# Optimization experiments

Measured on AMD Instinct MI355X. Metric: run time of the kernel, lower is better.

## Reference

```python
import jax, jax.numpy as jnp
import numpy as np


def setup_inputs() -> dict:
    key = jax.random.key(0)
    k0, k1, k2, k3 = jax.random.split(key, 4)
    B, N, C, Dout = 4, 8192, 64, 128
    coords = jax.random.normal(k0, (B, N, 3), dtype=jnp.float32)
    features = jax.random.normal(k1, (B, N, C), dtype=jnp.float32)
    W1 = jax.random.normal(k2, (C + 3, Dout), dtype=jnp.float32) / jnp.sqrt(jnp.float32(C + 3))
    b1 = jnp.zeros((Dout,), dtype=jnp.float32)
    W2 = jax.random.normal(k3, (Dout, Dout), dtype=jnp.float32) / jnp.sqrt(jnp.float32(Dout))
    b2 = jnp.zeros((Dout,), dtype=jnp.float32)
    return {"coords": coords, "features": features, "W1": W1, "b1": b1,
            "W2": W2, "b2": b2, "sample_count": 2048, "k": 32}


def reference(coords, features, W1, b1, W2, b2, sample_count, k):
    B, N, _ = coords.shape
    S = min(sample_count, N)
    kk = min(k, N)
    # deterministic linspace centroid sampling (same indices for every batch)
    idx = jnp.round(jnp.linspace(0.0, N - 1, S)).astype(jnp.int32)  # [S]
    sampled = coords[:, idx]  # [B,S,3]
    # squared distances via GEMM (same topk ordering as torch.cdist)
    s2 = jnp.sum(sampled * sampled, axis=-1)          # [B,S]
    c2 = jnp.sum(coords * coords, axis=-1)            # [B,N]
    d2 = s2[:, :, None] + c2[:, None, :] - 2.0 * jnp.einsum('bsd,bnd->bsn', sampled, coords)
    _, knn_idx = jax.lax.top_k(-d2, kk)               # [B,S,kk] smallest distances
    # per-batch irregular gathers
    grouped_c = jax.vmap(lambda c, i: c[i])(coords, knn_idx)      # [B,S,kk,3]
    rel = grouped_c - sampled[:, :, None, :]                      # relative coords
    grouped_f = jax.vmap(lambda f, i: f[i])(features, knn_idx)    # [B,S,kk,C]
    g = jnp.concatenate([rel, grouped_f], axis=-1)                # [B,S,kk,C+3]
    # shared MLP: Linear -> GELU(exact) -> Linear -> GELU(exact)
    h = jax.nn.gelu(g @ W1 + b1, approximate=False)
    h = jax.nn.gelu(h @ W2 + b2, approximate=False)
    pooled = jnp.max(h, axis=2)                                   # [B,S,Dout]
    return sampled, pooled
```

## Files before the change

kernel.cpp:

```cpp
#include <hip/hip_runtime.h>
#include <math.h>

typedef unsigned int u32;
typedef unsigned long long u64;
typedef float f32x2 __attribute__((ext_vector_type(2)));

#define BB 4
#define NN 8192
#define CC 64
#define DOUT 128
#define SS 2048
#define KSEL 32
#define CAPL 2048
#define CAP2 384
#define BREAK_CAP 128

__device__ __forceinline__ int sample_index(int s) {
    if (s == 1706) return 6826;
    const double step = 8191.0 / 2047.0;
    return (int)rint((double)s * step);
}

__device__ __forceinline__ u32 f2s(float f) {
    u32 u = __float_as_uint(f);
    return ((int)u < 0) ? ~u : (u ^ 0x80000000u);
}

__device__ __forceinline__ float gelu(float x) {
    return 0.5f * x * (1.0f + erff(x * 0.70710678118654752f));
}

__global__ __launch_bounds__(256)
__attribute__((amdgpu_waves_per_eu(5, 8)))
void k_select(const float* __restrict__ coords,
              float* __restrict__ out_sampled,
              int* __restrict__ selbuf,
              int selstride) {
    __shared__ __align__(16) u64 cand[CAPL];
    __shared__ __align__(16) u64 cand2[CAP2];
    __shared__ u32 wsum[32];
    __shared__ int sel[KSEL];
    __shared__ int s_nsel, s_ncand, s_n2;

    const int tid = threadIdx.x;
    const int lane = tid & 63;
    const int q = blockIdx.x;
    const int b = q >> 11;
    const int s = q & (SS - 1);
    const int si = sample_index(s);

    const float* cb = coords + (size_t)b * NN * 3;
    const float qx = cb[si * 3 + 0], qy = cb[si * 3 + 1], qz = cb[si * 3 + 2];
    const float q2 = __fadd_rn(__fadd_rn(__fmul_rn(qx, qx), __fmul_rn(qy, qy)), __fmul_rn(qz, qz));

    if (tid == 0) {
        float* dst = out_sampled + (size_t)q * 3;
        dst[0] = qx; dst[1] = qy; dst[2] = qz;
    }

    u32 kr[32];
#pragma unroll
    for (int i = 0; i < 32; i++) {
        int j = tid + (i << 8);
        float x = cb[j * 3 + 0], y = cb[j * 3 + 1], z = cb[j * 3 + 2];
        float n2 = __fadd_rn(__fadd_rn(__fmul_rn(x, x), __fmul_rn(y, y)), __fmul_rn(z, z));
        float dot = __fadd_rn(__fadd_rn(__fmul_rn(qx, x), __fmul_rn(qy, y)), __fmul_rn(qz, z));
        float d2 = __fsub_rn(__fadd_rn(q2, n2), __fmul_rn(2.0f, dot));
        kr[i] = f2s(d2);
    }

#define BFLY_WSUM()                                                          \
    _Pragma("unroll")                                                        \
    for (int w = 0; w < 8; w++) {                                            \
        _Pragma("unroll")                                                    \
        for (int d = 1; d < 64; d <<= 1) cnt[w] += __shfl_xor(cnt[w], d, 64);\
    }                                                                        \
    if ((tid & 63) == 0) {                                                   \
        int wv = tid >> 6;                                                   \
        _Pragma("unroll")                                                    \
        for (int w = 0; w < 8; w++) wsum[wv * 8 + w] = cnt[w];               \
    }                                                                        \
    __syncthreads();

#define SCAN_DIGIT()                                                         \
    u32 tot[8];                                                              \
    _Pragma("unroll")                                                        \
    for (int w = 0; w < 8; w++)                                              \
        tot[w] = wsum[w] + wsum[8 + w] + wsum[16 + w] + wsum[24 + w];        \
    run = 0; D = 15; cc = 0;                                                 \
    _Pragma("unroll")                                                        \
    for (int nib = 0; nib < 16; nib++) {                                     \
        int cv = (nib & 1) ? (int)(tot[nib >> 1] >> 16)                      \
                           : (int)(tot[nib >> 1] & 0xFFFFu);                 \
        if (base + run + cv >= KSEL) { D = nib; cc = cv; break; }            \
        run += cv;                                                           \
    }

    u32 pref = 0;
    int base = 0, shift = 28, c = 0;
    int p = 7;
    {
        u32 cnt[8] = {0, 0, 0, 0, 0, 0, 0, 0};
#pragma unroll
        for (int i = 0; i < 32; i++) {
            u32 nib = kr[i] >> 28;
            cnt[nib >> 1] += 1u << (16 * (nib & 1));
        }
        BFLY_WSUM()
        int run, D, cc;
        SCAN_DIGIT()
        base = run; pref = (u32)D << 28; c = cc;
        __syncthreads();
    }

    while (c > CAPL && p > 0) {
        p--;
        const int sh = 4 * p;
        const u32 hmask = 0xFFFFFFFFu << (sh + 4);
        u32 cnt[8] = {0, 0, 0, 0, 0, 0, 0, 0};
#pragma unroll
        for (int i = 0; i < 32; i++) {
            u32 kv = kr[i];
            if ((kv & hmask) == pref) {
                u32 nib = (kv >> sh) & 15u;
                cnt[nib >> 1] += 1u << (16 * (nib & 1));
            }
        }
        BFLY_WSUM()
        int run, D, cc;
        SCAN_DIGIT()
        base += run; pref |= (u32)D << sh; shift = sh; c = cc;
        __syncthreads();
    }

    if (tid == 0) { s_nsel = 0; s_ncand = 0; }
    __syncthreads();

    const u64 lmlt = (1ull << lane) - 1ull;
    {
        const u32 prefv = pref >> shift;
#pragma unroll
        for (int i = 0; i < 32; i++) {
            int j = tid + (i << 8);
            u32 kv = kr[i];
            u32 kp = kv >> shift;
            bool isS = kp < prefv;
            bool isC = kp == prefv;
            u64 bs = __ballot(isS);
            u64 bc = __ballot(isC);
            int basS = 0, basC = 0;
            if (lane == 0) {
                if (bs) basS = atomicAdd(&s_nsel, (int)__popcll(bs));
                if (bc) basC = atomicAdd(&s_ncand, (int)__popcll(bc));
            }
            basS = __shfl(basS, 0, 64);
            basC = __shfl(basC, 0, 64);
            if (isS) sel[basS + (int)__popcll(bs & lmlt)] = j;
            if (isC) {
                int pos = basC + (int)__popcll(bc & lmlt);
                if (pos < CAPL) cand[pos] = ((u64)kv << 32) | (u32)j;
            }
        }
    }
    __syncthreads();
    int nc = s_ncand; if (nc > CAPL) nc = CAPL;

    int p2 = shift >> 2;
    while (c > BREAK_CAP && p2 > 0) {
        p2--;
        const int sh = 4 * p2;
        const u32 ph = pref >> (sh + 4);
        u32 cnt[8] = {0, 0, 0, 0, 0, 0, 0, 0};
        for (int e = tid; e < nc; e += 256) {
            u32 kv = (u32)(cand[e] >> 32);
            if ((kv >> (sh + 4)) == ph) {
                u32 nib = (kv >> sh) & 15u;
                cnt[nib >> 1] += 1u << (16 * (nib & 1));
            }
        }
        BFLY_WSUM()
        int run, D, cc;
        SCAN_DIGIT()
        base += run; pref |= (u32)D << sh; shift = sh; c = cc;
        __syncthreads();
    }
#undef BFLY_WSUM
#undef SCAN_DIGIT

    if (tid == 0) s_n2 = 0;
    __syncthreads();
    {
        const u32 pv = pref >> shift;
        for (int e = tid; e < nc; e += 256) {
            u64 ent = cand[e];
            u32 kp = (u32)(ent >> 32) >> shift;
            bool isS = kp < pv;
            bool isC = kp == pv;
            u64 bs = __ballot(isS);
            u64 bc = __ballot(isC);
            int basS = 0, basC = 0;
            if (lane == 0) {
                if (bs) basS = atomicAdd(&s_nsel, (int)__popcll(bs));
                if (bc) basC = atomicAdd(&s_n2, (int)__popcll(bc));
            }
            basS = __shfl(basS, 0, 64);
            basC = __shfl(basC, 0, 64);
            if (isS) sel[basS + (int)__popcll(bs & lmlt)] = (int)(ent & 0xFFFFFFFFu);
            if (isC) {
                int pos = basC + (int)__popcll(bc & lmlt);
                if (pos < CAP2) cand2[pos] = ent;
            }
        }
    }
    __syncthreads();

    {
        const int nles = s_nsel;
        const int need = KSEL - nles;
        int n2 = s_n2; if (n2 > CAP2) n2 = CAP2;
        for (int ci = tid; ci < n2; ci += 256) {
            u64 me = cand2[ci];
            int r = 0;
            for (int m = 0; m < n2; m++) r += (cand2[m] < me) ? 1 : 0;
            if (r < need) sel[nles + r] = (int)(me & 0xFFFFFFFFu);
        }
    }
    __syncthreads();

    if (tid < KSEL) selbuf[(size_t)q * selstride + tid] = sel[tid];
}

__global__ __launch_bounds__(512) void k_mlp(const float* __restrict__ coords,
                                             const float* __restrict__ features,
                                             const float* __restrict__ w1,
                                             const float* __restrict__ b1,
                                             const float* __restrict__ w2,
                                             const float* __restrict__ b2,
                                             const int* __restrict__ selbuf,
                                             int selstride,
                                             float* __restrict__ pooled) {
    __shared__ __align__(16) unsigned char smem[32768];
    float* g    = (float*)smem;
    float* h    = (float*)smem;
    float* part = (float*)smem;
    __shared__ int sel2[2][KSEL];

    const int tid = threadIdx.x;
    const int q0 = blockIdx.x << 1;
    const int b = q0 >> 11;
    const float* cb = coords + (size_t)b * NN * 3;

    if (tid < 2 * KSEL) {
        int hq = tid >> 5;
        sel2[hq][tid & 31] = selbuf[(size_t)(q0 + hq) * selstride + (tid & 31)];
    }
    __syncthreads();

    {
        const int hq = tid >> 8;
        const int t = tid & 255;
        const int s = (q0 + hq) & (SS - 1);
        const int si = sample_index(s);
        const float qx = cb[si * 3 + 0], qy = cb[si * 3 + 1], qz = cb[si * 3 + 2];
        const int nbr = (t >> 3) & 31;
        const int cl = t & 7;
        const int n = sel2[hq][nbr];
        const float* fb = features + ((size_t)b * NN + n) * CC;
        float* gq = g + hq * 2144;
#pragma unroll
        for (int m = 0; m < 9; m++) {
            int ch = cl + (m << 3);
            if (ch < 67) {
                float v;
                if (ch < 3) v = cb[n * 3 + ch] - ((ch == 0) ? qx : (ch == 1) ? qy : qz);
                else        v = fb[ch - 3];
                gq[ch * 32 + nbr] = v;
            }
        }
    }
    __syncthreads();

    const int lane = tid & 63;
    const int chb = __builtin_amdgcn_readfirstlane((tid >> 6) << 4);
    const int hq = lane >> 5;
    const int nb = lane & 31;

    f32x2 acc2[8];

    {
        const f32x2* br2 = (const f32x2*)(b1 + chb);
#pragma unroll
        for (int k = 0; k < 8; k++) acc2[k] = br2[k];
        const float* aA = g + hq * 2144 + nb;
        const float* w1p = w1 + chb;
        for (int c = 0; c < 67; c++) {
            float a = aA[c * 32];
            f32x2 av = {a, a};
            const f32x2* wr2 = (const f32x2*)(w1p + c * DOUT);
#pragma unroll
            for (int k = 0; k < 8; k++)
                acc2[k] = __builtin_elementwise_fma(av, wr2[k], acc2[k]);
        }
    }
    __syncthreads();
    {
        float* hp = h + hq * 4096 + nb;
#pragma unroll
        for (int k = 0; k < 8; k++) {
            hp[(chb + 2 * k) * 32]     = gelu(acc2[k].x);
            hp[(chb + 2 * k + 1) * 32] = gelu(acc2[k].y);
        }
    }
    __syncthreads();

    {
        const f32x2* br2 = (const f32x2*)(b2 + chb);
#pragma unroll
        for (int k = 0; k < 8; k++) acc2[k] = br2[k];
        const float* aA = h + hq * 4096 + nb;
        const float* w2p = w2 + chb;
        for (int c = 0; c < DOUT; c++) {
            float a = aA[c * 32];
            f32x2 av = {a, a};
            const f32x2* wr2 = (const f32x2*)(w2p + c * DOUT);
#pragma unroll
            for (int k = 0; k < 8; k++)
                acc2[k] = __builtin_elementwise_fma(av, wr2[k], acc2[k]);
        }
    }
    __syncthreads();
    {
        float* pp = part + hq * 4096;
#pragma unroll
        for (int k = 0; k < 8; k++) {
            int j0 = chb + 2 * k;
            int j1 = j0 + 1;
            pp[j0 * 32 + (nb ^ (j0 & 31))] = acc2[k].x;
            pp[j1 * 32 + (nb ^ (j1 & 31))] = acc2[k].y;
        }
    }
    __syncthreads();

    if (tid < 256) {
        const int hq2 = tid >> 7;
        const int ch = tid & 127;
        const float* pr = part + hq2 * 4096 + ch * 32;
        const int sw = ch & 31;
        float mx = pr[0 ^ sw];
        float mn = mx;
#pragma unroll
        for (int w = 1; w < 32; w++) {
            float v = pr[w ^ sw];
            mx = fmaxf(mx, v);
            mn = fminf(mn, v);
        }
        pooled[(size_t)(q0 + hq2) * DOUT + ch] = fmaxf(gelu(mx), gelu(mn));
    }
}

extern "C" void kernel_launch(void* const* d_in, const int* in_sizes, int n_in,
                              void* d_out, int out_size, void* d_ws, size_t ws_size,
                              hipStream_t stream) {
    const float* coords = nullptr;
    const float* features = nullptr;
    const float* W1 = nullptr;
    const float* b1 = nullptr;
    const float* W2 = nullptr;
    const float* b2 = nullptr;
    for (int i = 0; i < n_in; i++) {
        int sz = in_sizes[i];
        const float* p = (const float*)d_in[i];
        if      (sz == BB * NN * 3)     coords = p;
        else if (sz == BB * NN * CC)    features = p;
        else if (sz == (CC + 3) * DOUT) W1 = p;
        else if (sz == DOUT * DOUT)     W2 = p;
        else if (sz == DOUT)            { if (!b1) b1 = p; else b2 = p; }
    }

    float* out_sampled = (float*)d_out;
    float* out_pooled  = (float*)d_out + (size_t)BB * SS * 3;

    const size_t sel_bytes = (size_t)BB * SS * KSEL * sizeof(int);
    int* selbuf;
    int selstride;
    if (ws_size >= sel_bytes && d_ws != nullptr) {
        selbuf = (int*)d_ws;
        selstride = KSEL;
    } else {
        selbuf = (int*)out_pooled;
        selstride = DOUT;
    }

    k_select<<<dim3(BB * SS), dim3(256), 0, stream>>>(coords, out_sampled, selbuf, selstride);
    k_mlp<<<dim3((BB * SS) / 2), dim3(512), 0, stream>>>(coords, features, W1, b1, W2, b2,
                                                         selbuf, selstride, out_pooled);
}
```

Baseline: 393.9 us.

## Fuse kNN selection and MLP into one kernel handling two queries per block

Merges the radix-select kernel and the MLP kernel into a single 512-thread kernel that processes two query points per block. The coordinates are loaded once to compute distances for both queries, and each selection runs serially, writing neighbor indices straight into shared memory. This removes the global selection buffer round-trip and one launch. In exchange the selection phase runs twice in sequence with block-wide syncs, and the larger block with more registers may lower occupancy compared with the former 256-thread select kernel.

```diff
diff --git a/kernel.cpp b/kernel.cpp
--- a/kernel.cpp
+++ b/kernel.cpp
@@ -30,44 +30,55 @@
     return 0.5f * x * (1.0f + erff(x * 0.70710678118654752f));
 }
 
-__global__ __launch_bounds__(256)
-__attribute__((amdgpu_waves_per_eu(5, 8)))
-void k_select(const float* __restrict__ coords,
-              float* __restrict__ out_sampled,
-              int* __restrict__ selbuf,
-              int selstride) {
-    __shared__ __align__(16) u64 cand[CAPL];
-    __shared__ __align__(16) u64 cand2[CAP2];
-    __shared__ u32 wsum[32];
-    __shared__ int sel[KSEL];
+__global__ __launch_bounds__(512) void k_fused(const float* __restrict__ coords,
+                                               const float* __restrict__ features,
+                                               const float* __restrict__ w1,
+                                               const float* __restrict__ b1,
+                                               const float* __restrict__ w2,
+                                               const float* __restrict__ b2,
+                                               float* __restrict__ out_sampled,
+                                               float* __restrict__ pooled) {
+    __shared__ __align__(16) unsigned char smem[32768];
+    u64*   cand  = (u64*)smem;
+    u64*   cand2 = (u64*)(smem + 16384);
+    u32*   wsum  = (u32*)(smem + 19456);
+    float* g     = (float*)smem;
+    float* h     = (float*)smem;
+    float* part  = (float*)smem;
+    __shared__ int sel2[2][KSEL];
     __shared__ int s_nsel, s_ncand, s_n2;
 
     const int tid = threadIdx.x;
     const int lane = tid & 63;
-    const int q = blockIdx.x;
-    const int b = q >> 11;
-    const int s = q & (SS - 1);
-    const int si = sample_index(s);
-
+    const int q0 = blockIdx.x << 1;
+    const int b = q0 >> 11;
     const float* cb = coords + (size_t)b * NN * 3;
-    const float qx = cb[si * 3 + 0], qy = cb[si * 3 + 1], qz = cb[si * 3 + 2];
-    const float q2 = __fadd_rn(__fadd_rn(__fmul_rn(qx, qx), __fmul_rn(qy, qy)), __fmul_rn(qz, qz));
+
+    const int si0 = sample_index(q0 & (SS - 1));
+    const int si1 = sample_index((q0 + 1) & (SS - 1));
+    const float qx0 = cb[si0 * 3 + 0], qy0 = cb[si0 * 3 + 1], qz0 = cb[si0 * 3 + 2];
+    const float qx1 = cb[si1 * 3 + 0], qy1 = cb[si1 * 3 + 1], qz1 = cb[si1 * 3 + 2];
+    const float q20 = __fadd_rn(__fadd_rn(__fmul_rn(qx0, qx0), __fmul_rn(qy0, qy0)), __fmul_rn(qz0, qz0));
+    const float q21 = __fadd_rn(__fadd_rn(__fmul_rn(qx1, qx1), __fmul_rn(qy1, qy1)), __fmul_rn(qz1, qz1));
 
     if (tid == 0) {
-        float* dst = out_sampled + (size_t)q * 3;
-        dst[0] = qx; dst[1] = qy; dst[2] = qz;
-    }
-
-    u32 kr[32];
-#pragma unroll
-    for (int i = 0; i < 32; i++) {
-        int j = tid + (i << 8);
+        float* dst = out_sampled + (size_t)q0 * 3;
+        dst[0] = qx0; dst[1] = qy0; dst[2] = qz0;
+        dst[3] = qx1; dst[4] = qy1; dst[5] = qz1;
+    }
+
+    u32 kr0[16], kr1[16];
+#pragma unroll
+    for (int i = 0; i < 16; i++) {
+        int j = tid + (i << 9);
         float x = cb[j * 3 + 0], y = cb[j * 3 + 1], z = cb[j * 3 + 2];
         float n2 = __fadd_rn(__fadd_rn(__fmul_rn(x, x), __fmul_rn(y, y)), __fmul_rn(z, z));
-        float dot = __fadd_rn(__fadd_rn(__fmul_rn(qx, x), __fmul_rn(qy, y)), __fmul_rn(qz, z));
-        float d2 = __fsub_rn(__fadd_rn(q2, n2), __fmul_rn(2.0f, dot));
-        kr[i] = f2s(d2);
-    }
+        float dot0 = __fadd_rn(__fadd_rn(__fmul_rn(qx0, x), __fmul_rn(qy0, y)), __fmul_rn(qz0, z));
+        kr0[i] = f2s(__fsub_rn(__fadd_rn(q20, n2), __fmul_rn(2.0f, dot0)));
+        float dot1 = __fadd_rn(__fadd_rn(__fmul_rn(qx1, x), __fmul_rn(qy1, y)), __fmul_rn(qz1, z));
+        kr1[i] = f2s(__fsub_rn(__fadd_rn(q21, n2), __fmul_rn(2.0f, dot1)));
+    }
+    const u64 lmlt = (1ull << lane) - 1ull;
 
 #define BFLY_WSUM()                                                          \
     _Pragma("unroll")                                                        \
@@ -85,8 +96,12 @@
 #define SCAN_DIGIT()                                                         \
     u32 tot[8];                                                              \
     _Pragma("unroll")                                                        \
-    for (int w = 0; w < 8; w++)                                              \
-        tot[w] = wsum[w] + wsum[8 + w] + wsum[16 + w] + wsum[24 + w];        \
+    for (int w = 0; w < 8; w++) {                                            \
+        u32 t = 0;                                                           \
+        _Pragma("unroll")                                                    \
+        for (int v = 0; v < 8; v++) t += wsum[v * 8 + w];                    \
+        tot[w] = t;                                                          \
+    }                                                                        \
     run = 0; D = 15; cc = 0;                                                 \
     _Pragma("unroll")                                                        \
     for (int nib = 0; nib < 16; nib++) {                                     \
@@ -96,172 +111,145 @@
         run += cv;                                                           \
     }
 
-    u32 pref = 0;
-    int base = 0, shift = 28, c = 0;
-    int p = 7;
-    {
-        u32 cnt[8] = {0, 0, 0, 0, 0, 0, 0, 0};
-#pragma unroll
-        for (int i = 0; i < 32; i++) {
-            u32 nib = kr[i] >> 28;
-            cnt[nib >> 1] += 1u << (16 * (nib & 1));
-        }
-        BFLY_WSUM()
-        int run, D, cc;
-        SCAN_DIGIT()
-        base = run; pref = (u32)D << 28; c = cc;
-        __syncthreads();
-    }
-
-    while (c > CAPL && p > 0) {
-        p--;
-        const int sh = 4 * p;
-        const u32 hmask = 0xFFFFFFFFu << (sh + 4);
-        u32 cnt[8] = {0, 0, 0, 0, 0, 0, 0, 0};
-#pragma unroll
-        for (int i = 0; i < 32; i++) {
-            u32 kv = kr[i];
-            if ((kv & hmask) == pref) {
-                u32 nib = (kv >> sh) & 15u;
-                cnt[nib >> 1] += 1u << (16 * (nib & 1));
-            }
-        }
-        BFLY_WSUM()
-        int run, D, cc;
-        SCAN_DIGIT()
-        base += run; pref |= (u32)D << sh; shift = sh; c = cc;
-        __syncthreads();
-    }
-
-    if (tid == 0) { s_nsel = 0; s_ncand = 0; }
-    __syncthreads();
-
-    const u64 lmlt = (1ull << lane) - 1ull;
-    {
-        const u32 prefv = pref >> shift;
-#pragma unroll
-        for (int i = 0; i < 32; i++) {
-            int j = tid + (i << 8);
-            u32 kv = kr[i];
-            u32 kp = kv >> shift;
-            bool isS = kp < prefv;
-            bool isC = kp == prefv;
-            u64 bs = __ballot(isS);
-            u64 bc = __ballot(isC);
-            int basS = 0, basC = 0;
-            if (lane == 0) {
-                if (bs) basS = atomicAdd(&s_nsel, (int)__popcll(bs));
-                if (bc) basC = atomicAdd(&s_ncand, (int)__popcll(bc));
-            }
-            basS = __shfl(basS, 0, 64);
-            basC = __shfl(basC, 0, 64);
-            if (isS) sel[basS + (int)__popcll(bs & lmlt)] = j;
-            if (isC) {
-                int pos = basC + (int)__popcll(bc & lmlt);
-                if (pos < CAPL) cand[pos] = ((u64)kv << 32) | (u32)j;
-            }
-        }
-    }
-    __syncthreads();
-    int nc = s_ncand; if (nc > CAPL) nc = CAPL;
-
-    int p2 = shift >> 2;
-    while (c > BREAK_CAP && p2 > 0) {
-        p2--;
-        const int sh = 4 * p2;
-        const u32 ph = pref >> (sh + 4);
-        u32 cnt[8] = {0, 0, 0, 0, 0, 0, 0, 0};
-        for (int e = tid; e < nc; e += 256) {
-            u32 kv = (u32)(cand[e] >> 32);
-            if ((kv >> (sh + 4)) == ph) {
-                u32 nib = (kv >> sh) & 15u;
-                cnt[nib >> 1] += 1u << (16 * (nib & 1));
-            }
-        }
-        BFLY_WSUM()
-        int run, D, cc;
-        SCAN_DIGIT()
-        base += run; pref |= (u32)D << sh; shift = sh; c = cc;
-        __syncthreads();
-    }
+#define SELECT_Q(KR, ROW)                                                    \
+{                                                                            \
+    u32 pref = 0;                                                            \
+    int base = 0, shift = 28, c = 0;                                         \
+    int p = 7;                                                               \
+    {                                                                        \
+        u32 cnt[8] = {0, 0, 0, 0, 0, 0, 0, 0};                               \
+        _Pragma("unroll")                                                    \
+        for (int i = 0; i < 16; i++) {                                       \
+            u32 nib = KR[i] >> 28;                                           \
+            cnt[nib >> 1] += 1u << (16 * (nib & 1));                         \
+        }                                                                    \
+        BFLY_WSUM()                                                          \
+        int run, D, cc;                                                      \
+        SCAN_DIGIT()                                                         \
+        base = run; pref = (u32)D << 28; c = cc;                             \
+        __syncthreads();                                                     \
+    }                                                                        \
+    while (c > CAPL && p > 0) {                                              \
+        p--;                                                                 \
+        const int sh = 4 * p;                                                \
+        const u32 hmask = 0xFFFFFFFFu << (sh + 4);                           \
+        u32 cnt[8] = {0, 0, 0, 0, 0, 0, 0, 0};                               \
+        _Pragma("unroll")                                                    \
+        for (int i = 0; i < 16; i++) {                                       \
+            u32 kv = KR[i];                                                  \
+            if ((kv & hmask) == pref) {                                      \
+                u32 nib = (kv >> sh) & 15u;                                  \
+                cnt[nib >> 1] += 1u << (16 * (nib & 1));                     \
+            }                                                                \
+        }                                                                    \
+        BFLY_WSUM()                                                          \
+        int run, D, cc;                                                      \
+        SCAN_DIGIT()                                                         \
+        base += run; pref |= (u32)D << sh; shift = sh; c = cc;               \
+        __syncthreads();                                                     \
+    }                                                                        \
+    if (tid == 0) { s_nsel = 0; s_ncand = 0; }                               \
+    __syncthreads();                                                         \
+    {                                                                        \
+        const u32 prefv = pref >> shift;                                     \
+        _Pragma("unroll")                                                    \
+        for (int i = 0; i < 16; i++) {                                       \
+            int j = tid + (i << 9);                                          \
+            u32 kv = KR[i];                                                  \
+            u32 kp = kv >> shift;                                            \
+            bool isS = kp < prefv;                                           \
+            bool isC = kp == prefv;                                          \
+            u64 bs = __ballot(isS);                                          \
+            u64 bc = __ballot(isC);                                          \
+            int basS = 0, basC = 0;                                          \
+            if (lane == 0) {                                                 \
+                if (bs) basS = atomicAdd(&s_nsel, (int)__popcll(bs));        \
+                if (bc) basC = atomicAdd(&s_ncand, (int)__popcll(bc));       \
+            }                                                                \
+            basS = __shfl(basS, 0, 64);                                      \
+            basC = __shfl(basC, 0, 64);                                      \
+            if (isS) sel2[ROW][basS + (int)__popcll(bs & lmlt)] = j;         \
+            if (isC) {                                                       \
+                int pos = basC + (int)__popcll(bc & lmlt);                   \
+                if (pos < CAPL) cand[pos] = ((u64)kv << 32) | (u32)j;        \
+            }                                                                \
+        }                                                                    \
+    }                                                                        \
+    __syncthreads();                                                         \
+    int nc = s_ncand; if (nc > CAPL) nc = CAPL;                              \
+    int p2 = shift >> 2;                                                     \
+    while (c > BREAK_CAP && p2 > 0) {                                        \
+        p2--;                                                                \
+        const int sh = 4 * p2;                                               \
+        const u32 ph = pref >> (sh + 4);                                     \
+        u32 cnt[8] = {0, 0, 0, 0, 0, 0, 0, 0};                               \
+        for (int e = tid; e < nc; e += 512) {                                \
+            u32 kv = (u32)(cand[e] >> 32);                                   \
+            if ((kv >> (sh + 4)) == ph) {                                    \
+                u32 nib = (kv >> sh) & 15u;                                  \
+                cnt[nib >> 1] += 1u << (16 * (nib & 1));                     \
+            }                                                                \
+        }                                                                    \
+        BFLY_WSUM()                                                          \
+        int run, D, cc;                                                      \
+        SCAN_DIGIT()                                                         \
+        base += run; pref |= (u32)D << sh; shift = sh; c = cc;               \
+        __syncthreads();                                                     \
+    }                                                                        \
+    if (tid == 0) s_n2 = 0;                                                  \
+    __syncthreads();                                                         \
+    {                                                                        \
+        const u32 pv = pref >> shift;                                        \
+        for (int e = tid; e < nc; e += 512) {                                \
+            u64 ent = cand[e];                                               \
+            u32 kp = (u32)(ent >> 32) >> shift;                              \
+            bool isS = kp < pv;                                              \
+            bool isC = kp == pv;                                             \
+            u64 bs = __ballot(isS);                                          \
+            u64 bc = __ballot(isC);                                          \
+            int basS = 0, basC = 0;                                          \
+            if (lane == 0) {                                                 \
+                if (bs) basS = atomicAdd(&s_nsel, (int)__popcll(bs));        \
+                if (bc) basC = atomicAdd(&s_n2, (int)__popcll(bc));          \
+            }                                                                \
+            basS = __shfl(basS, 0, 64);                                      \
+            basC = __shfl(basC, 0, 64);                                      \
+            if (isS) sel2[ROW][basS + (int)__popcll(bs & lmlt)] =            \
+                (int)(ent & 0xFFFFFFFFu);                                    \
+            if (isC) {                                                       \
+                int pos = basC + (int)__popcll(bc & lmlt);                   \
+                if (pos < CAP2) cand2[pos] = ent;                            \
+            }                                                                \
+        }                                                                    \
+    }                                                                        \
+    __syncthreads();                                                         \
+    {                                                                        \
+        const int nles = s_nsel;                                             \
+        const int need = KSEL - nles;                                        \
+        int n2 = s_n2; if (n2 > CAP2) n2 = CAP2;                             \
+        for (int ci = tid; ci < n2; ci += 512) {                             \
+            u64 me = cand2[ci];                                              \
+            int r = 0;                                                       \
+            for (int m = 0; m < n2; m++) r += (cand2[m] < me) ? 1 : 0;       \
+            if (r < need) sel2[ROW][nles + r] = (int)(me & 0xFFFFFFFFu);     \
+        }                                                                    \
+    }                                                                        \
+    __syncthreads();                                                         \
+}
+
+    SELECT_Q(kr0, 0)
+    SELECT_Q(kr1, 1)
+
+#undef SELECT_Q
 #undef BFLY_WSUM
 #undef SCAN_DIGIT
 
-    if (tid == 0) s_n2 = 0;
-    __syncthreads();
-    {
-        const u32 pv = pref >> shift;
-        for (int e = tid; e < nc; e += 256) {
-            u64 ent = cand[e];
-            u32 kp = (u32)(ent >> 32) >> shift;
-            bool isS = kp < pv;
-            bool isC = kp == pv;
-            u64 bs = __ballot(isS);
-            u64 bc = __ballot(isC);
-            int basS = 0, basC = 0;
-            if (lane == 0) {
-                if (bs) basS = atomicAdd(&s_nsel, (int)__popcll(bs));
-                if (bc) basC = atomicAdd(&s_n2, (int)__popcll(bc));
-            }
-            basS = __shfl(basS, 0, 64);
-            basC = __shfl(basC, 0, 64);
-            if (isS) sel[basS + (int)__popcll(bs & lmlt)] = (int)(ent & 0xFFFFFFFFu);
-            if (isC) {
-                int pos = basC + (int)__popcll(bc & lmlt);
-                if (pos < CAP2) cand2[pos] = ent;
-            }
-        }
-    }
-    __syncthreads();
-
-    {
-        const int nles = s_nsel;
-        const int need = KSEL - nles;
-        int n2 = s_n2; if (n2 > CAP2) n2 = CAP2;
-        for (int ci = tid; ci < n2; ci += 256) {
-            u64 me = cand2[ci];
-            int r = 0;
-            for (int m = 0; m < n2; m++) r += (cand2[m] < me) ? 1 : 0;
-            if (r < need) sel[nles + r] = (int)(me & 0xFFFFFFFFu);
-        }
-    }
-    __syncthreads();
-
-    if (tid < KSEL) selbuf[(size_t)q * selstride + tid] = sel[tid];
-}
-
-__global__ __launch_bounds__(512) void k_mlp(const float* __restrict__ coords,
-                                             const float* __restrict__ features,
-                                             const float* __restrict__ w1,
-                                             const float* __restrict__ b1,
-                                             const float* __restrict__ w2,
-                                             const float* __restrict__ b2,
-                                             const int* __restrict__ selbuf,
-                                             int selstride,
-                                             float* __restrict__ pooled) {
-    __shared__ __align__(16) unsigned char smem[32768];
-    float* g    = (float*)smem;
-    float* h    = (float*)smem;
-    float* part = (float*)smem;
-    __shared__ int sel2[2][KSEL];
-
-    const int tid = threadIdx.x;
-    const int q0 = blockIdx.x << 1;
-    const int b = q0 >> 11;
-    const float* cb = coords + (size_t)b * NN * 3;
-
-    if (tid < 2 * KSEL) {
-        int hq = tid >> 5;
-        sel2[hq][tid & 31] = selbuf[(size_t)(q0 + hq) * selstride + (tid & 31)];
-    }
-    __syncthreads();
-
     {
         const int hq = tid >> 8;
+        const float qxh = hq ? qx1 : qx0;
+        const float qyh = hq ? qy1 : qy0;
+        const float qzh = hq ? qz1 : qz0;
         const int t = tid & 255;
-        const int s = (q0 + hq) & (SS - 1);
-        const int si = sample_index(s);
-        const float qx = cb[si * 3 + 0], qy = cb[si * 3 + 1], qz = cb[si * 3 + 2];
         const int nbr = (t >> 3) & 31;
         const int cl = t & 7;
         const int n = sel2[hq][nbr];
@@ -272,7 +260,7 @@
             int ch = cl + (m << 3);
             if (ch < 67) {
                 float v;
-                if (ch < 3) v = cb[n * 3 + ch] - ((ch == 0) ? qx : (ch == 1) ? qy : qz);
+                if (ch < 3) v = cb[n * 3 + ch] - ((ch == 0) ? qxh : (ch == 1) ? qyh : qzh);
                 else        v = fb[ch - 3];
                 gq[ch * 32 + nbr] = v;
             }
@@ -280,7 +268,6 @@
     }
     __syncthreads();
 
-    const int lane = tid & 63;
     const int chb = __builtin_amdgcn_readfirstlane((tid >> 6) << 4);
     const int hq = lane >> 5;
     const int nb = lane & 31;
@@ -380,18 +367,6 @@
     float* out_sampled = (float*)d_out;
     float* out_pooled  = (float*)d_out + (size_t)BB * SS * 3;
 
-    const size_t sel_bytes = (size_t)BB * SS * KSEL * sizeof(int);
-    int* selbuf;
-    int selstride;
-    if (ws_size >= sel_bytes && d_ws != nullptr) {
-        selbuf = (int*)d_ws;
-        selstride = KSEL;
-    } else {
-        selbuf = (int*)out_pooled;
-        selstride = DOUT;
-    }
-
-    k_select<<<dim3(BB * SS), dim3(256), 0, stream>>>(coords, out_sampled, selbuf, selstride);
-    k_mlp<<<dim3((BB * SS) / 2), dim3(512), 0, stream>>>(coords, features, W1, b1, W2, b2,
-                                                         selbuf, selstride, out_pooled);
-}
+    k_fused<<<dim3((BB * SS) / 2), dim3(512), 0, stream>>>(coords, features, W1, b1, W2, b2,
+                                                           out_sampled, out_pooled);
+}
```

After: 729.3 us. +85.1%, slower.
